# Performance work log

Hardware: AMD Instinct MI355X
Metric: run time of the kernel (lower is better)

## Reference

```python
import jax, jax.numpy as jnp
import numpy as np

H = 256          # hidden_size
S = 4            # feature size (2D -> 4)
T_OUT = 16       # args.output // args.skip
HT_LIM = 100.0   # hardtanh limit
B = 16384
OBS = 16


def lstm_cell(x, h, c, Wih, Whh, bih, bhh):
    # PyTorch gate order: i, f, g, o
    g = x @ Wih.T + h @ Whh.T + bih + bhh  # [B, 4H]
    i, f, gg, o = jnp.split(g, 4, axis=-1)
    c = jax.nn.sigmoid(f) * c + jax.nn.sigmoid(i) * jnp.tanh(gg)
    h = jax.nn.sigmoid(o) * jnp.tanh(c)
    return h, c


def encode(seq, Wih, Whh, bih, bhh):
    # seq: [B, T, S]; single-layer LSTM, return final (h, c)
    h0 = jnp.zeros((seq.shape[0], H), seq.dtype)
    def step(carry, x):
        h, c = carry
        return lstm_cell(x, h, c, Wih, Whh, bih, bhh), None
    (h, c), _ = jax.lax.scan(step, (h0, h0), jnp.swapaxes(seq, 0, 1))
    return h, c


def setup_inputs() -> dict:
    key = jax.random.key(0)
    ks = jax.random.split(key, 32)
    sc = 0.05
    def W(k, shape):
        return (jax.random.normal(k, shape, jnp.float32) * sc)
    inp = {
        'speed': jax.random.normal(ks[0], (B, OBS, S), jnp.float32),
        'pos': jax.random.normal(ks[1], (B, OBS, S), jnp.float32),
        # speed encoder LSTM
        'sp_Wih': W(ks[2], (4 * H, S)), 'sp_Whh': W(ks[3], (4 * H, H)),
        'sp_bih': W(ks[4], (4 * H,)), 'sp_bhh': W(ks[5], (4 * H,)),
        # pos encoder LSTM
        'po_Wih': W(ks[6], (4 * H, S)), 'po_Whh': W(ks[7], (4 * H, H)),
        'po_bih': W(ks[8], (4 * H,)), 'po_bhh': W(ks[9], (4 * H,)),
        # speed decoder LSTMCell
        'dsp_Wih': W(ks[10], (4 * H, S)), 'dsp_Whh': W(ks[11], (4 * H, H)),
        'dsp_bih': W(ks[12], (4 * H,)), 'dsp_bhh': W(ks[13], (4 * H,)),
        # crossing decoder LSTMCell
        'dcr_Wih': W(ks[14], (4 * H, S)), 'dcr_Whh': W(ks[15], (4 * H, H)),
        'dcr_bih': W(ks[16], (4 * H,)), 'dcr_bhh': W(ks[17], (4 * H,)),
        # heads
        'fc_speed_W': W(ks[18], (S, H)), 'fc_speed_b': W(ks[19], (S,)),
        'fc_cross_W': W(ks[20], (2, H)), 'fc_cross_b': W(ks[21], (2,)),
        'emb_W': W(ks[22], (S, H)), 'emb_b': W(ks[23], (S,)),
    }
    return inp


def reference(speed, pos,
              sp_Wih, sp_Whh, sp_bih, sp_bhh,
              po_Wih, po_Whh, po_bih, po_bhh,
              dsp_Wih, dsp_Whh, dsp_bih, dsp_bhh,
              dcr_Wih, dcr_Whh, dcr_bih, dcr_bhh,
              fc_speed_W, fc_speed_b, fc_cross_W, fc_cross_b,
              emb_W, emb_b):
    hsp, csp = encode(speed, sp_Wih, sp_Whh, sp_bih, sp_bhh)
    hpo, cpo = encode(pos, po_Wih, po_Whh, po_bih, po_bhh)
    h0 = hpo + hsp
    c0 = cpo + csp

    # ---- speed decoder: feed back hardtanh(fc_speed(h)) (detached) ----
    def sp_step(carry, _):
        h, c, x = carry
        h, c = lstm_cell(x, h, c, dsp_Wih, dsp_Whh, dsp_bih, dsp_bhh)
        out = jnp.clip(h @ fc_speed_W.T + fc_speed_b, -HT_LIM, HT_LIM)
        return (h, c, jax.lax.stop_gradient(out)), out
    _, sp_outs = jax.lax.scan(sp_step, (h0, c0, speed[:, -1, :]), None, length=T_OUT)
    speed_outputs = jnp.swapaxes(sp_outs, 0, 1)  # [B, T_OUT, S]

    # ---- crossing decoder: feed back relu(pos_embedding(h)) (detached) ----
    def cr_step(carry, _):
        h, c, x = carry
        h, c = lstm_cell(x, h, c, dcr_Wih, dcr_Whh, dcr_bih, dcr_bhh)
        logits = jax.nn.relu(h @ fc_cross_W.T + fc_cross_b)  # [B, 2]
        out = jax.nn.softmax(logits, axis=1)
        x_next = jax.lax.stop_gradient(jax.nn.relu(h @ emb_W.T + emb_b))
        return (h, c, x_next), out
    _, cr_outs = jax.lax.scan(cr_step, (h0, c0, pos[:, -1, :]), None, length=T_OUT)
    crossing_outputs = jnp.swapaxes(cr_outs, 0, 1)  # [B, T_OUT, 2]

    return (speed_outputs, crossing_outputs)
```

## Files before the change

kernel.cpp:

```cpp
#include <hip/hip_runtime.h>

typedef unsigned short ushort_t;
typedef __bf16 bf16x8 __attribute__((ext_vector_type(8)));
typedef float f32x4 __attribute__((ext_vector_type(4)));

#define PACK_W_ELEMS (8*9*8*512)
#define HEAD_ELEMS   (9*512)
#define PACK_TOTAL   (4*PACK_W_ELEMS + 2*HEAD_ELEMS)
#define FLAG_OFS     PACK_TOTAL

__device__ __forceinline__ float bf2f(ushort_t u){ return __uint_as_float(((unsigned)u)<<16); }
__device__ __forceinline__ ushort_t f2bf(float f){
  __bf16 h = (__bf16)f;
  return *(ushort_t*)&h;
}
__device__ __forceinline__ float rcp_(float x){ return __builtin_amdgcn_rcpf(x); }
__device__ __forceinline__ float sigmf_(float x){ return rcp_(1.0f + __expf(-x)); }
__device__ __forceinline__ float tanhf_(float x){ return 1.0f - 2.0f*rcp_(1.0f + __expf(2.0f*x)); }

__device__ __forceinline__ int sniff_f32(const ushort_t* w){
  int f32 = 0;
  #pragma unroll
  for (int i = 0; i < 32; ++i){
    float f = bf2f(w[2*i]);
    if (!(f > -8.f && f < 8.f)) f32 = 1;
  }
  return f32;
}
__device__ __forceinline__ float ldin(const ushort_t* p, int i, int f32){
  return f32 ? ((const float*)p)[i] : bf2f(p[i]);
}
__device__ __forceinline__ ushort_t ldw(const ushort_t* p, int i, int f32){
  return f32 ? f2bf(((const float*)p)[i]) : p[i];
}

struct PackArgs {
  const ushort_t* wih[4]; const ushort_t* whh[4];
  const ushort_t* bih[4]; const ushort_t* bhh[4];
  const ushort_t* fcsp_w; const ushort_t* fcsp_b;
  const ushort_t* fccr_w; const ushort_t* fccr_b;
  const ushort_t* emb_w;  const ushort_t* emb_b;
  ushort_t* ws;
};

__global__ void pack_kernel(PackArgs a){
  const int f32 = sniff_f32(a.whh[0]);
  int idx = blockIdx.x*256 + threadIdx.x;
  if (blockIdx.x == 0 && threadIdx.x == 0) *(int*)(a.ws + FLAG_OFS) = f32;
  const int total_w = 4*PACK_W_ELEMS;
  if (idx < total_w){
    int l = idx / PACK_W_ELEMS;
    int r = idx % PACK_W_ELEMS;
    int j = r & 7;
    int lane = (r>>3) & 63;
    int tile = r >> 9;
    int gu = tile & 7;
    int kt = (tile >> 3) % 9;
    int wv = tile / 72;
    int g = gu >> 1, u = gu & 1;
    int n = (g*16 + wv*2 + u)*16 + (lane & 15);
    int k = kt*32 + ((lane>>4)<<3) + j;
    ushort_t v = 0;
    if (k < 256)       v = ldw(a.whh[l], n*256 + k, f32);
    else if (k < 260)  v = ldw(a.wih[l], n*4 + (k-256), f32);
    else if (k == 260) v = f2bf(ldin(a.bih[l], n, f32) + ldin(a.bhh[l], n, f32));
    a.ws[l*PACK_W_ELEMS + r] = v;
    return;
  }
  idx -= total_w;
  if (idx < 2*HEAD_ELEMS){
    int which = idx / HEAD_ELEMS;
    int r = idx % HEAD_ELEMS;
    int j = r & 7; int lane = (r>>3)&63; int kt = r>>9;
    int n = lane & 15; int k = kt*32 + ((lane>>4)<<3) + j;
    ushort_t v = 0;
    if (which == 0){
      if (n < 4){
        if (k < 256)       v = ldw(a.fcsp_w, n*256 + k, f32);
        else if (k == 260) v = f2bf(ldin(a.fcsp_b, n, f32));
      }
    } else {
      if (n < 4){
        if (k < 256)       v = ldw(a.emb_w, n*256 + k, f32);
        else if (k == 260) v = f2bf(ldin(a.emb_b, n, f32));
      } else if (n < 6){
        if (k < 256)       v = ldw(a.fccr_w, (n-4)*256 + k, f32);
        else if (k == 260) v = f2bf(ldin(a.fccr_b, n-4, f32));
      }
    }
    a.ws[total_w + idx] = v;
  }
}

#define PRE4(bw, s0, s1, s2, s3)                \
  bf16x8 s0 = *(const bf16x8*)&(bw)[0*512];     \
  bf16x8 s1 = *(const bf16x8*)&(bw)[1*512];     \
  bf16x8 s2 = *(const bf16x8*)&(bw)[2*512];     \
  bf16x8 s3 = *(const bf16x8*)&(bw)[3*512];

__device__ __forceinline__ void gate_gemm(const ushort_t* __restrict__ Aln,
                                          const ushort_t* __restrict__ bw,
                                          f32x4 (&acc)[4][8], int lane,
                                          bf16x8 p0, bf16x8 p1, bf16x8 p2, bf16x8 p3){
  #pragma unroll
  for (int i = 0; i < 4; ++i)
    #pragma unroll
    for (int j = 0; j < 8; ++j) acc[i][j] = (f32x4){0.f,0.f,0.f,0.f};
  const ushort_t* bp = bw;
  #pragma unroll 1
  for (int kt = 0; kt < 9; ++kt){
    bf16x8 q0 = *(const bf16x8*)&bp[4*512];
    bf16x8 q1 = *(const bf16x8*)&bp[5*512];
    bf16x8 q2 = *(const bf16x8*)&bp[6*512];
    bf16x8 q3 = *(const bf16x8*)&bp[7*512];
    bf16x8 a0 = *(const bf16x8*)&Aln[(0*9+kt)*512];
    bf16x8 a1 = *(const bf16x8*)&Aln[(1*9+kt)*512];
    bf16x8 a2 = *(const bf16x8*)&Aln[(2*9+kt)*512];
    bf16x8 a3 = *(const bf16x8*)&Aln[(3*9+kt)*512];
    acc[0][0] = __builtin_amdgcn_mfma_f32_16x16x32_bf16(a0, p0, acc[0][0], 0, 0, 0);
    acc[1][0] = __builtin_amdgcn_mfma_f32_16x16x32_bf16(a1, p0, acc[1][0], 0, 0, 0);
    acc[2][0] = __builtin_amdgcn_mfma_f32_16x16x32_bf16(a2, p0, acc[2][0], 0, 0, 0);
    acc[3][0] = __builtin_amdgcn_mfma_f32_16x16x32_bf16(a3, p0, acc[3][0], 0, 0, 0);
    acc[0][1] = __builtin_amdgcn_mfma_f32_16x16x32_bf16(a0, p1, acc[0][1], 0, 0, 0);
    acc[1][1] = __builtin_amdgcn_mfma_f32_16x16x32_bf16(a1, p1, acc[1][1], 0, 0, 0);
    acc[2][1] = __builtin_amdgcn_mfma_f32_16x16x32_bf16(a2, p1, acc[2][1], 0, 0, 0);
    acc[3][1] = __builtin_amdgcn_mfma_f32_16x16x32_bf16(a3, p1, acc[3][1], 0, 0, 0);
    acc[0][2] = __builtin_amdgcn_mfma_f32_16x16x32_bf16(a0, p2, acc[0][2], 0, 0, 0);
    acc[1][2] = __builtin_amdgcn_mfma_f32_16x16x32_bf16(a1, p2, acc[1][2], 0, 0, 0);
    acc[2][2] = __builtin_amdgcn_mfma_f32_16x16x32_bf16(a2, p2, acc[2][2], 0, 0, 0);
    acc[3][2] = __builtin_amdgcn_mfma_f32_16x16x32_bf16(a3, p2, acc[3][2], 0, 0, 0);
    acc[0][3] = __builtin_amdgcn_mfma_f32_16x16x32_bf16(a0, p3, acc[0][3], 0, 0, 0);
    acc[1][3] = __builtin_amdgcn_mfma_f32_16x16x32_bf16(a1, p3, acc[1][3], 0, 0, 0);
    acc[2][3] = __builtin_amdgcn_mfma_f32_16x16x32_bf16(a2, p3, acc[2][3], 0, 0, 0);
    acc[3][3] = __builtin_amdgcn_mfma_f32_16x16x32_bf16(a3, p3, acc[3][3], 0, 0, 0);
    if (kt < 8){
      p0 = *(const bf16x8*)&bp[4096 + 0*512];
      p1 = *(const bf16x8*)&bp[4096 + 1*512];
      p2 = *(const bf16x8*)&bp[4096 + 2*512];
      p3 = *(const bf16x8*)&bp[4096 + 3*512];
    }
    acc[0][4] = __builtin_amdgcn_mfma_f32_16x16x32_bf16(a0, q0, acc[0][4], 0, 0, 0);
    acc[1][4] = __builtin_amdgcn_mfma_f32_16x16x32_bf16(a1, q0, acc[1][4], 0, 0, 0);
    acc[2][4] = __builtin_amdgcn_mfma_f32_16x16x32_bf16(a2, q0, acc[2][4], 0, 0, 0);
    acc[3][4] = __builtin_amdgcn_mfma_f32_16x16x32_bf16(a3, q0, acc[3][4], 0, 0, 0);
    acc[0][5] = __builtin_amdgcn_mfma_f32_16x16x32_bf16(a0, q1, acc[0][5], 0, 0, 0);
    acc[1][5] = __builtin_amdgcn_mfma_f32_16x16x32_bf16(a1, q1, acc[1][5], 0, 0, 0);
    acc[2][5] = __builtin_amdgcn_mfma_f32_16x16x32_bf16(a2, q1, acc[2][5], 0, 0, 0);
    acc[3][5] = __builtin_amdgcn_mfma_f32_16x16x32_bf16(a3, q1, acc[3][5], 0, 0, 0);
    acc[0][6] = __builtin_amdgcn_mfma_f32_16x16x32_bf16(a0, q2, acc[0][6], 0, 0, 0);
    acc[1][6] = __builtin_amdgcn_mfma_f32_16x16x32_bf16(a1, q2, acc[1][6], 0, 0, 0);
    acc[2][6] = __builtin_amdgcn_mfma_f32_16x16x32_bf16(a2, q2, acc[2][6], 0, 0, 0);
    acc[3][6] = __builtin_amdgcn_mfma_f32_16x16x32_bf16(a3, q2, acc[3][6], 0, 0, 0);
    acc[0][7] = __builtin_amdgcn_mfma_f32_16x16x32_bf16(a0, q3, acc[0][7], 0, 0, 0);
    acc[1][7] = __builtin_amdgcn_mfma_f32_16x16x32_bf16(a1, q3, acc[1][7], 0, 0, 0);
    acc[2][7] = __builtin_amdgcn_mfma_f32_16x16x32_bf16(a2, q3, acc[2][7], 0, 0, 0);
    acc[3][7] = __builtin_amdgcn_mfma_f32_16x16x32_bf16(a3, q3, acc[3][7], 0, 0, 0);
    bp += 4096;
  }
}

__device__ __forceinline__ void gates_wb(f32x4 (&acc)[4][8], float (&cw)[4][2][4],
                                         ushort_t* __restrict__ Ap, int wbBase){
  #pragma unroll
  for (int mt = 0; mt < 4; ++mt)
    #pragma unroll
    for (int u = 0; u < 2; ++u)
      #pragma unroll
      for (int r = 0; r < 4; ++r){
        const float i_ = acc[mt][u][r];
        const float f_ = acc[mt][2+u][r];
        const float g_ = acc[mt][4+u][r];
        const float o_ = acc[mt][6+u][r];
        const float ei = __expf(-i_);
        const float ef = __expf(-f_);
        const float eg = __expf(-2.0f*g_);
        const float di = 1.0f + ei, df = 1.0f + ef;
        const float dg = 1.0f + eg, ng = 1.0f - eg;
        const float dig = di*dg;
        const float cn = (cw[mt][u][r]*dig + ng*df) * rcp_(df*dig);
        const float eo = __expf(-o_);
        const float ec = __expf(-2.0f*cn);
        const float hn = (1.0f - ec) * rcp_((1.0f + eo)*(1.0f + ec));
        cw[mt][u][r] = cn;
        Ap[mt*4608 + u*256 + r*8 + wbBase] = f2bf(hn);
      }
}

__global__ __launch_bounds__(512, 2) void pvlstm_main(
    const ushort_t* __restrict__ ws,
    const ushort_t* __restrict__ speed,
    const ushort_t* __restrict__ pos,
    void* __restrict__ outv)
{
  __shared__ ushort_t ApS[4*9*512];
  __shared__ ushort_t ApP[4*9*512];
  __shared__ ushort_t xsS[64*64];
  __shared__ ushort_t xsP[64*64];
  __shared__ float    ostS[64*64];
  __shared__ float    ostC[64*32];

  const int f32   = *(const int*)(ws + FLAG_OFS);
  const int tid   = threadIdx.x;
  const int lane  = tid & 63;
  const int w     = tid >> 6;
  const int col16 = lane & 15;
  const int quad  = lane >> 4;
  const int brow0 = blockIdx.x * 64;
  const int wbBase = w*512 + (col16>>3)*128 + quad*32 + (col16&7);

  ushort_t* outu = (ushort_t*)outv;
  float*    outf = (float*)outv;

  const ushort_t* headsp = ws + 4*PACK_W_ELEMS;
  const ushort_t* headcr = headsp + HEAD_ELEMS;
  const ushort_t* aS  = ApS + lane*8;
  const ushort_t* aP  = ApP + lane*8;
  const ushort_t* bwS  = ws + 0*PACK_W_ELEMS + (size_t)w*36864 + (size_t)lane*8;
  const ushort_t* bwP  = ws + 1*PACK_W_ELEMS + (size_t)w*36864 + (size_t)lane*8;
  const ushort_t* bwDS = ws + 2*PACK_W_ELEMS + (size_t)w*36864 + (size_t)lane*8;
  const ushort_t* bwDC = ws + 3*PACK_W_ELEMS + (size_t)w*36864 + (size_t)lane*8;

  float cwA[4][2][4], cwB[4][2][4];
  f32x4 acc[4][8];

  for (int i = tid; i < 4096; i += 512){
    int gi = (brow0 + (i>>6))*64 + (i&63);
    xsS[i] = f2bf(ldin(speed, gi, f32));
    xsP[i] = f2bf(ldin(pos,   gi, f32));
  }
  for (int i = tid; i < 4*9*512/2; i += 512){
    ((unsigned*)ApS)[i] = 0u; ((unsigned*)ApP)[i] = 0u;
  }
  #pragma unroll
  for (int mt = 0; mt < 4; ++mt)
    #pragma unroll
    for (int u = 0; u < 2; ++u)
      #pragma unroll
      for (int r = 0; r < 4; ++r){ cwA[mt][u][r] = 0.f; cwB[mt][u][r] = 0.f; }
  __syncthreads();
  if (tid < 64){
    ushort_t* xpS = &ApS[((tid>>4)*9 + 8)*512 + (tid&15)*8];
    ushort_t* xpP = &ApP[((tid>>4)*9 + 8)*512 + (tid&15)*8];
    *(uint2*)xpS = *(const uint2*)&xsS[tid*64];
    xpS[4] = (ushort_t)0x3f80;
    xpP[4] = (ushort_t)0x3f80;
  }
  __syncthreads();

  for (int t = 0; t < 16; ++t){
    {
      PRE4(bwS, s0, s1, s2, s3)
      if (t > 0) gates_wb(acc, cwB, ApP, wbBase);
      if (tid < 64)
        *(uint2*)&ApP[((tid>>4)*9 + 8)*512 + (tid&15)*8] = *(const uint2*)&xsP[tid*64 + t*4];
      gate_gemm(aS, bwS, acc, lane, s0, s1, s2, s3);
    }
    __syncthreads();
    {
      PRE4(bwP, s0, s1, s2, s3)
      gates_wb(acc, cwA, ApS, wbBase);
      if (t < 15 && tid < 64)
        *(uint2*)&ApS[((tid>>4)*9 + 8)*512 + (tid&15)*8] = *(const uint2*)&xsS[tid*64 + t*4 + 4];
      gate_gemm(aP, bwP, acc, lane, s0, s1, s2, s3);
    }
    __syncthreads();
  }
  #pragma unroll
  for (int mt = 0; mt < 4; ++mt)
    #pragma unroll
    for (int u = 0; u < 2; ++u)
      #pragma unroll
      for (int r = 0; r < 4; ++r){
        const float i_ = acc[mt][u][r];
        const float f_ = acc[mt][2+u][r];
        const float g_ = acc[mt][4+u][r];
        const float o_ = acc[mt][6+u][r];
        const float ei = __expf(-i_);
        const float ef = __expf(-f_);
        const float eg = __expf(-2.0f*g_);
        const float di = 1.0f + ei, df = 1.0f + ef;
        const float dg = 1.0f + eg, ng = 1.0f - eg;
        const float dig = di*dg;
        const float cn = (cwB[mt][u][r]*dig + ng*df) * rcp_(df*dig);
        const float eo = __expf(-o_);
        const float ec = __expf(-2.0f*cn);
        const float hn = (1.0f - ec) * rcp_((1.0f + eo)*(1.0f + ec));
        const float c0 = cwA[mt][u][r] + cn;
        cwA[mt][u][r] = c0; cwB[mt][u][r] = c0;
        const int ad = mt*4608 + u*256 + r*8 + wbBase;
        ushort_t h0 = f2bf(bf2f(ApS[ad]) + hn);
        ApS[ad] = h0; ApP[ad] = h0;
      }
  if (tid < 64){
    *(uint2*)&ApS[((tid>>4)*9 + 8)*512 + (tid&15)*8] = *(const uint2*)&xsS[tid*64 + 60];
    *(uint2*)&ApP[((tid>>4)*9 + 8)*512 + (tid&15)*8] = *(const uint2*)&xsP[tid*64 + 60];
  }
  __syncthreads();

  for (int t = 0; t < 16; ++t){
    {
      PRE4(bwDS, s0, s1, s2, s3)
      if (t > 0 && w >= 4){
        const int mt = w - 4;
        f32x4 hacc = (f32x4){0.f,0.f,0.f,0.f};
        #pragma unroll
        for (int kt = 0; kt < 9; ++kt){
          bf16x8 a  = *(const bf16x8*)&aP[(mt*9+kt)*512];
          bf16x8 bv = *(const bf16x8*)&headcr[((size_t)kt*64 + lane)*8];
          hacc = __builtin_amdgcn_mfma_f32_16x16x32_bf16(a, bv, hacc, 0, 0, 0);
        }
        const int s = col16;
        #pragma unroll
        for (int r = 0; r < 4; ++r){
          float v = fmaxf(hacc[r], 0.f);
          const float o = __shfl_xor(v, 1, 64);
          const int m = mt*16 + quad*4 + r;
          if (s < 4){
            ApP[(mt*9+8)*512 + (m&15)*8 + s] = f2bf(v);
          } else if (s < 6){
            const float mx = fmaxf(v, o);
            const float e0 = __expf(v-mx), e1 = __expf(o-mx);
            ostC[m*32 + (t-1)*2 + (s-4)] = e0*rcp_(e0+e1);
          }
        }
      }
      gate_gemm(aS, bwDS, acc, lane, s0, s1, s2, s3);
    }
    __syncthreads();
    {
      PRE4(bwDC, s0, s1, s2, s3)
      gates_wb(acc, cwA, ApS, wbBase);
      gate_gemm(aP, bwDC, acc, lane, s0, s1, s2, s3);
    }
    __syncthreads();
    gates_wb(acc, cwB, ApP, wbBase);
    if (w < 4){
      const int mt = w;
      f32x4 hacc = (f32x4){0.f,0.f,0.f,0.f};
      #pragma unroll
      for (int kt = 0; kt < 9; ++kt){
        bf16x8 a  = *(const bf16x8*)&aS[(mt*9+kt)*512];
        bf16x8 bv = *(const bf16x8*)&headsp[((size_t)kt*64 + lane)*8];
        hacc = __builtin_amdgcn_mfma_f32_16x16x32_bf16(a, bv, hacc, 0, 0, 0);
      }
      const int s = col16;
      if (s < 4){
        #pragma unroll
        for (int r = 0; r < 4; ++r){
          float v = fminf(fmaxf(hacc[r], -100.f), 100.f);
          const int m = mt*16 + quad*4 + r;
          ostS[m*64 + t*4 + s] = v;
          ApS[(mt*9+8)*512 + (m&15)*8 + s] = f2bf(v);
        }
      }
    }
    __syncthreads();
  }
  if (w >= 4){
    const int mt = w - 4;
    f32x4 hacc = (f32x4){0.f,0.f,0.f,0.f};
    #pragma unroll
    for (int kt = 0; kt < 9; ++kt){
      bf16x8 a  = *(const bf16x8*)&aP[(mt*9+kt)*512];
      bf16x8 bv = *(const bf16x8*)&headcr[((size_t)kt*64 + lane)*8];
      hacc = __builtin_amdgcn_mfma_f32_16x16x32_bf16(a, bv, hacc, 0, 0, 0);
    }
    const int s = col16;
    if (s >= 4 && s < 6){
      #pragma unroll
      for (int r = 0; r < 4; ++r){
        float v = fmaxf(hacc[r], 0.f);
        const float o = __shfl_xor(v, 1, 64);
        const int m = mt*16 + quad*4 + r;
        const float mx = fmaxf(v, o);
        const float e0 = __expf(v-mx), e1 = __expf(o-mx);
        ostC[m*32 + 15*2 + (s-4)] = e0*rcp_(e0+e1);
      }
    }
  }
  __syncthreads();

  for (int i = tid; i < 4096; i += 512){
    const int oi = (brow0 + (i>>6))*64 + (i&63);
    const float v = ostS[i];
    if (f32) outf[oi] = v; else outu[oi] = f2bf(v);
  }
  for (int i = tid; i < 2048; i += 512){
    const int oi = 1048576 + (brow0 + (i>>5))*32 + (i&31);
    const float v = ostC[i];
    if (f32) outf[oi] = v; else outu[oi] = f2bf(v);
  }
}

extern "C" void kernel_launch(void* const* d_in, const int* in_sizes, int n_in,
                              void* d_out, int out_size, void* d_ws, size_t ws_size,
                              hipStream_t stream) {
  PackArgs pa;
  pa.wih[0]=(const ushort_t*)d_in[2];  pa.whh[0]=(const ushort_t*)d_in[3];
  pa.bih[0]=(const ushort_t*)d_in[4];  pa.bhh[0]=(const ushort_t*)d_in[5];
  pa.wih[1]=(const ushort_t*)d_in[6];  pa.whh[1]=(const ushort_t*)d_in[7];
  pa.bih[1]=(const ushort_t*)d_in[8];  pa.bhh[1]=(const ushort_t*)d_in[9];
  pa.wih[2]=(const ushort_t*)d_in[10]; pa.whh[2]=(const ushort_t*)d_in[11];
  pa.bih[2]=(const ushort_t*)d_in[12]; pa.bhh[2]=(const ushort_t*)d_in[13];
  pa.wih[3]=(const ushort_t*)d_in[14]; pa.whh[3]=(const ushort_t*)d_in[15];
  pa.bih[3]=(const ushort_t*)d_in[16]; pa.bhh[3]=(const ushort_t*)d_in[17];
  pa.fcsp_w=(const ushort_t*)d_in[18]; pa.fcsp_b=(const ushort_t*)d_in[19];
  pa.fccr_w=(const ushort_t*)d_in[20]; pa.fccr_b=(const ushort_t*)d_in[21];
  pa.emb_w =(const ushort_t*)d_in[22]; pa.emb_b =(const ushort_t*)d_in[23];
  pa.ws = (ushort_t*)d_ws;

  hipLaunchKernelGGL(pack_kernel, dim3((PACK_TOTAL + 255)/256), dim3(256), 0, stream, pa);
  hipLaunchKernelGGL(pvlstm_main, dim3(256), dim3(512), 0, stream,
      (const ushort_t*)d_ws,
      (const ushort_t*)d_in[0], (const ushort_t*)d_in[1],
      d_out);
}
```

Before: 827.4 us.

## Switch gate GEMMs from 16x16x32 to 32x32x16 MFMA with repacked layouts

Replaces the 16x16x32 bf16 MFMA tiling of the LSTM gate GEMMs with 32x32x16 MFMA tiles, repacking weights and the shared-memory hidden-state layout to match. Each wave now owns 2x4 accumulators of 16 floats over 18 K-steps instead of 4x8 accumulators of 4 floats over 9 K-steps. The aim is fewer MFMA issues and fewer A/B fragment loads per output. The head GEMMs, gate writeback and input-feed addressing are remapped to the new layout, which risks indexing errors and different LDS bank-conflict patterns.

```diff
diff --git a/kernel.cpp b/kernel.cpp
--- a/kernel.cpp
+++ b/kernel.cpp
@@ -3,8 +3,9 @@
 typedef unsigned short ushort_t;
 typedef __bf16 bf16x8 __attribute__((ext_vector_type(8)));
 typedef float f32x4 __attribute__((ext_vector_type(4)));
-
-#define PACK_W_ELEMS (8*9*8*512)
+typedef float f32x16 __attribute__((ext_vector_type(16)));
+
+#define PACK_W_ELEMS (8*18*4*512)
 #define HEAD_ELEMS   (9*512)
 #define PACK_TOTAL   (4*PACK_W_ELEMS + 2*HEAD_ELEMS)
 #define FLAG_OFS     PACK_TOTAL
@@ -15,8 +16,6 @@
   return *(ushort_t*)&h;
 }
 __device__ __forceinline__ float rcp_(float x){ return __builtin_amdgcn_rcpf(x); }
-__device__ __forceinline__ float sigmf_(float x){ return rcp_(1.0f + __expf(-x)); }
-__device__ __forceinline__ float tanhf_(float x){ return 1.0f - 2.0f*rcp_(1.0f + __expf(2.0f*x)); }
 
 __device__ __forceinline__ int sniff_f32(const ushort_t* w){
   int f32 = 0;
@@ -54,12 +53,11 @@
     int j = r & 7;
     int lane = (r>>3) & 63;
     int tile = r >> 9;
-    int gu = tile & 7;
-    int kt = (tile >> 3) % 9;
+    int g = tile & 3;
+    int kt = (tile >> 2) % 18;
     int wv = tile / 72;
-    int g = gu >> 1, u = gu & 1;
-    int n = (g*16 + wv*2 + u)*16 + (lane & 15);
-    int k = kt*32 + ((lane>>4)<<3) + j;
+    int n = g*256 + wv*32 + (lane & 31);
+    int k = kt*16 + ((lane>>5)<<3) + j;
     ushort_t v = 0;
     if (k < 256)       v = ldw(a.whh[l], n*256 + k, f32);
     else if (k < 260)  v = ldw(a.wih[l], n*4 + (k-256), f32);
@@ -100,90 +98,61 @@
 
 __device__ __forceinline__ void gate_gemm(const ushort_t* __restrict__ Aln,
                                           const ushort_t* __restrict__ bw,
-                                          f32x4 (&acc)[4][8], int lane,
+                                          f32x16 (&acc)[2][4],
                                           bf16x8 p0, bf16x8 p1, bf16x8 p2, bf16x8 p3){
   #pragma unroll
-  for (int i = 0; i < 4; ++i)
-    #pragma unroll
-    for (int j = 0; j < 8; ++j) acc[i][j] = (f32x4){0.f,0.f,0.f,0.f};
+  for (int i = 0; i < 2; ++i)
+    #pragma unroll
+    for (int j = 0; j < 4; ++j) acc[i][j] = (f32x16)(0.f);
   const ushort_t* bp = bw;
   #pragma unroll 1
-  for (int kt = 0; kt < 9; ++kt){
-    bf16x8 q0 = *(const bf16x8*)&bp[4*512];
-    bf16x8 q1 = *(const bf16x8*)&bp[5*512];
-    bf16x8 q2 = *(const bf16x8*)&bp[6*512];
-    bf16x8 q3 = *(const bf16x8*)&bp[7*512];
-    bf16x8 a0 = *(const bf16x8*)&Aln[(0*9+kt)*512];
-    bf16x8 a1 = *(const bf16x8*)&Aln[(1*9+kt)*512];
-    bf16x8 a2 = *(const bf16x8*)&Aln[(2*9+kt)*512];
-    bf16x8 a3 = *(const bf16x8*)&Aln[(3*9+kt)*512];
-    acc[0][0] = __builtin_amdgcn_mfma_f32_16x16x32_bf16(a0, p0, acc[0][0], 0, 0, 0);
-    acc[1][0] = __builtin_amdgcn_mfma_f32_16x16x32_bf16(a1, p0, acc[1][0], 0, 0, 0);
-    acc[2][0] = __builtin_amdgcn_mfma_f32_16x16x32_bf16(a2, p0, acc[2][0], 0, 0, 0);
-    acc[3][0] = __builtin_amdgcn_mfma_f32_16x16x32_bf16(a3, p0, acc[3][0], 0, 0, 0);
-    acc[0][1] = __builtin_amdgcn_mfma_f32_16x16x32_bf16(a0, p1, acc[0][1], 0, 0, 0);
-    acc[1][1] = __builtin_amdgcn_mfma_f32_16x16x32_bf16(a1, p1, acc[1][1], 0, 0, 0);
-    acc[2][1] = __builtin_amdgcn_mfma_f32_16x16x32_bf16(a2, p1, acc[2][1], 0, 0, 0);
-    acc[3][1] = __builtin_amdgcn_mfma_f32_16x16x32_bf16(a3, p1, acc[3][1], 0, 0, 0);
-    acc[0][2] = __builtin_amdgcn_mfma_f32_16x16x32_bf16(a0, p2, acc[0][2], 0, 0, 0);
-    acc[1][2] = __builtin_amdgcn_mfma_f32_16x16x32_bf16(a1, p2, acc[1][2], 0, 0, 0);
-    acc[2][2] = __builtin_amdgcn_mfma_f32_16x16x32_bf16(a2, p2, acc[2][2], 0, 0, 0);
-    acc[3][2] = __builtin_amdgcn_mfma_f32_16x16x32_bf16(a3, p2, acc[3][2], 0, 0, 0);
-    acc[0][3] = __builtin_amdgcn_mfma_f32_16x16x32_bf16(a0, p3, acc[0][3], 0, 0, 0);
-    acc[1][3] = __builtin_amdgcn_mfma_f32_16x16x32_bf16(a1, p3, acc[1][3], 0, 0, 0);
-    acc[2][3] = __builtin_amdgcn_mfma_f32_16x16x32_bf16(a2, p3, acc[2][3], 0, 0, 0);
-    acc[3][3] = __builtin_amdgcn_mfma_f32_16x16x32_bf16(a3, p3, acc[3][3], 0, 0, 0);
-    if (kt < 8){
-      p0 = *(const bf16x8*)&bp[4096 + 0*512];
-      p1 = *(const bf16x8*)&bp[4096 + 1*512];
-      p2 = *(const bf16x8*)&bp[4096 + 2*512];
-      p3 = *(const bf16x8*)&bp[4096 + 3*512];
-    }
-    acc[0][4] = __builtin_amdgcn_mfma_f32_16x16x32_bf16(a0, q0, acc[0][4], 0, 0, 0);
-    acc[1][4] = __builtin_amdgcn_mfma_f32_16x16x32_bf16(a1, q0, acc[1][4], 0, 0, 0);
-    acc[2][4] = __builtin_amdgcn_mfma_f32_16x16x32_bf16(a2, q0, acc[2][4], 0, 0, 0);
-    acc[3][4] = __builtin_amdgcn_mfma_f32_16x16x32_bf16(a3, q0, acc[3][4], 0, 0, 0);
-    acc[0][5] = __builtin_amdgcn_mfma_f32_16x16x32_bf16(a0, q1, acc[0][5], 0, 0, 0);
-    acc[1][5] = __builtin_amdgcn_mfma_f32_16x16x32_bf16(a1, q1, acc[1][5], 0, 0, 0);
-    acc[2][5] = __builtin_amdgcn_mfma_f32_16x16x32_bf16(a2, q1, acc[2][5], 0, 0, 0);
-    acc[3][5] = __builtin_amdgcn_mfma_f32_16x16x32_bf16(a3, q1, acc[3][5], 0, 0, 0);
-    acc[0][6] = __builtin_amdgcn_mfma_f32_16x16x32_bf16(a0, q2, acc[0][6], 0, 0, 0);
-    acc[1][6] = __builtin_amdgcn_mfma_f32_16x16x32_bf16(a1, q2, acc[1][6], 0, 0, 0);
-    acc[2][6] = __builtin_amdgcn_mfma_f32_16x16x32_bf16(a2, q2, acc[2][6], 0, 0, 0);
-    acc[3][6] = __builtin_amdgcn_mfma_f32_16x16x32_bf16(a3, q2, acc[3][6], 0, 0, 0);
-    acc[0][7] = __builtin_amdgcn_mfma_f32_16x16x32_bf16(a0, q3, acc[0][7], 0, 0, 0);
-    acc[1][7] = __builtin_amdgcn_mfma_f32_16x16x32_bf16(a1, q3, acc[1][7], 0, 0, 0);
-    acc[2][7] = __builtin_amdgcn_mfma_f32_16x16x32_bf16(a2, q3, acc[2][7], 0, 0, 0);
-    acc[3][7] = __builtin_amdgcn_mfma_f32_16x16x32_bf16(a3, q3, acc[3][7], 0, 0, 0);
-    bp += 4096;
-  }
-}
-
-__device__ __forceinline__ void gates_wb(f32x4 (&acc)[4][8], float (&cw)[4][2][4],
-                                         ushort_t* __restrict__ Ap, int wbBase){
-  #pragma unroll
-  for (int mt = 0; mt < 4; ++mt)
-    #pragma unroll
-    for (int u = 0; u < 2; ++u)
-      #pragma unroll
-      for (int r = 0; r < 4; ++r){
-        const float i_ = acc[mt][u][r];
-        const float f_ = acc[mt][2+u][r];
-        const float g_ = acc[mt][4+u][r];
-        const float o_ = acc[mt][6+u][r];
-        const float ei = __expf(-i_);
-        const float ef = __expf(-f_);
-        const float eg = __expf(-2.0f*g_);
-        const float di = 1.0f + ei, df = 1.0f + ef;
-        const float dg = 1.0f + eg, ng = 1.0f - eg;
-        const float dig = di*dg;
-        const float cn = (cw[mt][u][r]*dig + ng*df) * rcp_(df*dig);
-        const float eo = __expf(-o_);
-        const float ec = __expf(-2.0f*cn);
-        const float hn = (1.0f - ec) * rcp_((1.0f + eo)*(1.0f + ec));
-        cw[mt][u][r] = cn;
-        Ap[mt*4608 + u*256 + r*8 + wbBase] = f2bf(hn);
-      }
+  for (int kt = 0; kt < 18; ++kt){
+    bf16x8 a0 = *(const bf16x8*)&Aln[(     kt)*512];
+    bf16x8 a1 = *(const bf16x8*)&Aln[(18 + kt)*512];
+    acc[0][0] = __builtin_amdgcn_mfma_f32_32x32x16_bf16(a0, p0, acc[0][0], 0, 0, 0);
+    acc[1][0] = __builtin_amdgcn_mfma_f32_32x32x16_bf16(a1, p0, acc[1][0], 0, 0, 0);
+    acc[0][1] = __builtin_amdgcn_mfma_f32_32x32x16_bf16(a0, p1, acc[0][1], 0, 0, 0);
+    acc[1][1] = __builtin_amdgcn_mfma_f32_32x32x16_bf16(a1, p1, acc[1][1], 0, 0, 0);
+    bf16x8 q0, q1, q2, q3;
+    if (kt < 17){
+      q0 = *(const bf16x8*)&bp[2048 + 0*512];
+      q1 = *(const bf16x8*)&bp[2048 + 1*512];
+      q2 = *(const bf16x8*)&bp[2048 + 2*512];
+      q3 = *(const bf16x8*)&bp[2048 + 3*512];
+    }
+    acc[0][2] = __builtin_amdgcn_mfma_f32_32x32x16_bf16(a0, p2, acc[0][2], 0, 0, 0);
+    acc[1][2] = __builtin_amdgcn_mfma_f32_32x32x16_bf16(a1, p2, acc[1][2], 0, 0, 0);
+    acc[0][3] = __builtin_amdgcn_mfma_f32_32x32x16_bf16(a0, p3, acc[0][3], 0, 0, 0);
+    acc[1][3] = __builtin_amdgcn_mfma_f32_32x32x16_bf16(a1, p3, acc[1][3], 0, 0, 0);
+    if (kt < 17){ p0 = q0; p1 = q1; p2 = q2; p3 = q3; }
+    bp += 2048;
+  }
+}
+
+__device__ __forceinline__ void gates_wb(f32x16 (&acc)[2][4], float (&cw)[2][16],
+                                         ushort_t* __restrict__ Ap, int wbBase, int hi5){
+  #pragma unroll
+  for (int mt = 0; mt < 2; ++mt)
+    #pragma unroll
+    for (int reg = 0; reg < 16; ++reg){
+      const float i_ = acc[mt][0][reg];
+      const float f_ = acc[mt][1][reg];
+      const float g_ = acc[mt][2][reg];
+      const float o_ = acc[mt][3][reg];
+      const float ei = __expf(-i_);
+      const float ef = __expf(-f_);
+      const float eg = __expf(-2.0f*g_);
+      const float di = 1.0f + ei, df = 1.0f + ef;
+      const float dg = 1.0f + eg, ng = 1.0f - eg;
+      const float dig = di*dg;
+      const float cn = (cw[mt][reg]*dig + ng*df) * rcp_(df*dig);
+      const float eo = __expf(-o_);
+      const float ec = __expf(-2.0f*cn);
+      const float hn = (1.0f - ec) * rcp_((1.0f + eo)*(1.0f + ec));
+      cw[mt][reg] = cn;
+      const int rw = (reg&3) + 8*(reg>>2) + 4*hi5;
+      Ap[mt*9216 + wbBase + rw*8] = f2bf(hn);
+    }
 }
 
 __global__ __launch_bounds__(512, 2) void pvlstm_main(
@@ -192,8 +161,8 @@
     const ushort_t* __restrict__ pos,
     void* __restrict__ outv)
 {
-  __shared__ ushort_t ApS[4*9*512];
-  __shared__ ushort_t ApP[4*9*512];
+  __shared__ ushort_t ApS[2*18*512];
+  __shared__ ushort_t ApP[2*18*512];
   __shared__ ushort_t xsS[64*64];
   __shared__ ushort_t xsP[64*64];
   __shared__ float    ostS[64*64];
@@ -205,8 +174,10 @@
   const int w     = tid >> 6;
   const int col16 = lane & 15;
   const int quad  = lane >> 4;
+  const int c5    = lane & 31;
+  const int hi5   = lane >> 5;
   const int brow0 = blockIdx.x * 64;
-  const int wbBase = w*512 + (col16>>3)*128 + quad*32 + (col16&7);
+  const int wbBase = (w*2 + (c5>>4))*512 + ((c5>>3)&1)*256 + (lane & 7);
 
   ushort_t* outu = (ushort_t*)outv;
   float*    outf = (float*)outv;
@@ -220,27 +191,25 @@
   const ushort_t* bwDS = ws + 2*PACK_W_ELEMS + (size_t)w*36864 + (size_t)lane*8;
   const ushort_t* bwDC = ws + 3*PACK_W_ELEMS + (size_t)w*36864 + (size_t)lane*8;
 
-  float cwA[4][2][4], cwB[4][2][4];
-  f32x4 acc[4][8];
+  float cwA[2][16], cwB[2][16];
+  f32x16 acc[2][4];
 
   for (int i = tid; i < 4096; i += 512){
     int gi = (brow0 + (i>>6))*64 + (i&63);
     xsS[i] = f2bf(ldin(speed, gi, f32));
     xsP[i] = f2bf(ldin(pos,   gi, f32));
   }
-  for (int i = tid; i < 4*9*512/2; i += 512){
+  for (int i = tid; i < 2*18*512/2; i += 512){
     ((unsigned*)ApS)[i] = 0u; ((unsigned*)ApP)[i] = 0u;
   }
   #pragma unroll
-  for (int mt = 0; mt < 4; ++mt)
-    #pragma unroll
-    for (int u = 0; u < 2; ++u)
-      #pragma unroll
-      for (int r = 0; r < 4; ++r){ cwA[mt][u][r] = 0.f; cwB[mt][u][r] = 0.f; }
+  for (int mt = 0; mt < 2; ++mt)
+    #pragma unroll
+    for (int r = 0; r < 16; ++r){ cwA[mt][r] = 0.f; cwB[mt][r] = 0.f; }
   __syncthreads();
   if (tid < 64){
-    ushort_t* xpS = &ApS[((tid>>4)*9 + 8)*512 + (tid&15)*8];
-    ushort_t* xpP = &ApP[((tid>>4)*9 + 8)*512 + (tid&15)*8];
+    ushort_t* xpS = &ApS[((tid>>5)*18 + 16)*512 + (tid&31)*8];
+    ushort_t* xpP = &ApP[((tid>>5)*18 + 16)*512 + (tid&31)*8];
     *(uint2*)xpS = *(const uint2*)&xsS[tid*64];
     xpS[4] = (ushort_t)0x3f80;
     xpP[4] = (ushort_t)0x3f80;
@@ -250,50 +219,49 @@
   for (int t = 0; t < 16; ++t){
     {
       PRE4(bwS, s0, s1, s2, s3)
-      if (t > 0) gates_wb(acc, cwB, ApP, wbBase);
+      if (t > 0) gates_wb(acc, cwB, ApP, wbBase, hi5);
       if (tid < 64)
-        *(uint2*)&ApP[((tid>>4)*9 + 8)*512 + (tid&15)*8] = *(const uint2*)&xsP[tid*64 + t*4];
-      gate_gemm(aS, bwS, acc, lane, s0, s1, s2, s3);
+        *(uint2*)&ApP[((tid>>5)*18 + 16)*512 + (tid&31)*8] = *(const uint2*)&xsP[tid*64 + t*4];
+      gate_gemm(aS, bwS, acc, s0, s1, s2, s3);
     }
     __syncthreads();
     {
       PRE4(bwP, s0, s1, s2, s3)
-      gates_wb(acc, cwA, ApS, wbBase);
+      gates_wb(acc, cwA, ApS, wbBase, hi5);
       if (t < 15 && tid < 64)
-        *(uint2*)&ApS[((tid>>4)*9 + 8)*512 + (tid&15)*8] = *(const uint2*)&xsS[tid*64 + t*4 + 4];
-      gate_gemm(aP, bwP, acc, lane, s0, s1, s2, s3);
-    }
-    __syncthreads();
-  }
-  #pragma unroll
-  for (int mt = 0; mt < 4; ++mt)
-    #pragma unroll
-    for (int u = 0; u < 2; ++u)
-      #pragma unroll
-      for (int r = 0; r < 4; ++r){
-        const float i_ = acc[mt][u][r];
-        const float f_ = acc[mt][2+u][r];
-        const float g_ = acc[mt][4+u][r];
-        const float o_ = acc[mt][6+u][r];
-        const float ei = __expf(-i_);
-        const float ef = __expf(-f_);
-        const float eg = __expf(-2.0f*g_);
-        const float di = 1.0f + ei, df = 1.0f + ef;
-        const float dg = 1.0f + eg, ng = 1.0f - eg;
-        const float dig = di*dg;
-        const float cn = (cwB[mt][u][r]*dig + ng*df) * rcp_(df*dig);
-        const float eo = __expf(-o_);
-        const float ec = __expf(-2.0f*cn);
-        const float hn = (1.0f - ec) * rcp_((1.0f + eo)*(1.0f + ec));
-        const float c0 = cwA[mt][u][r] + cn;
-        cwA[mt][u][r] = c0; cwB[mt][u][r] = c0;
-        const int ad = mt*4608 + u*256 + r*8 + wbBase;
-        ushort_t h0 = f2bf(bf2f(ApS[ad]) + hn);
-        ApS[ad] = h0; ApP[ad] = h0;
-      }
+        *(uint2*)&ApS[((tid>>5)*18 + 16)*512 + (tid&31)*8] = *(const uint2*)&xsS[tid*64 + t*4 + 4];
+      gate_gemm(aP, bwP, acc, s0, s1, s2, s3);
+    }
+    __syncthreads();
+  }
+  #pragma unroll
+  for (int mt = 0; mt < 2; ++mt)
+    #pragma unroll
+    for (int reg = 0; reg < 16; ++reg){
+      const float i_ = acc[mt][0][reg];
+      const float f_ = acc[mt][1][reg];
+      const float g_ = acc[mt][2][reg];
+      const float o_ = acc[mt][3][reg];
+      const float ei = __expf(-i_);
+      const float ef = __expf(-f_);
+      const float eg = __expf(-2.0f*g_);
+      const float di = 1.0f + ei, df = 1.0f + ef;
+      const float dg = 1.0f + eg, ng = 1.0f - eg;
+      const float dig = di*dg;
+      const float cn = (cwB[mt][reg]*dig + ng*df) * rcp_(df*dig);
+      const float eo = __expf(-o_);
+      const float ec = __expf(-2.0f*cn);
+      const float hn = (1.0f - ec) * rcp_((1.0f + eo)*(1.0f + ec));
+      const float c0 = cwA[mt][reg] + cn;
+      cwA[mt][reg] = c0; cwB[mt][reg] = c0;
+      const int rw = (reg&3) + 8*(reg>>2) + 4*hi5;
+      const int ad = mt*9216 + wbBase + rw*8;
+      ushort_t h0 = f2bf(bf2f(ApS[ad]) + hn);
+      ApS[ad] = h0; ApP[ad] = h0;
+    }
   if (tid < 64){
-    *(uint2*)&ApS[((tid>>4)*9 + 8)*512 + (tid&15)*8] = *(const uint2*)&xsS[tid*64 + 60];
-    *(uint2*)&ApP[((tid>>4)*9 + 8)*512 + (tid&15)*8] = *(const uint2*)&xsP[tid*64 + 60];
+    *(uint2*)&ApS[((tid>>5)*18 + 16)*512 + (tid&31)*8] = *(const uint2*)&xsS[tid*64 + 60];
+    *(uint2*)&ApP[((tid>>5)*18 + 16)*512 + (tid&31)*8] = *(const uint2*)&xsP[tid*64 + 60];
   }
   __syncthreads();
 
@@ -302,10 +270,11 @@
       PRE4(bwDS, s0, s1, s2, s3)
       if (t > 0 && w >= 4){
         const int mt = w - 4;
+        const int hbase = ((mt>>1)*18 + hi5)*512 + ((quad&1)*256) + ((mt&1)*16 + col16)*8;
         f32x4 hacc = (f32x4){0.f,0.f,0.f,0.f};
         #pragma unroll
         for (int kt = 0; kt < 9; ++kt){
-          bf16x8 a  = *(const bf16x8*)&aP[(mt*9+kt)*512];
+          bf16x8 a  = *(const bf16x8*)&ApP[hbase + kt*1024];
           bf16x8 bv = *(const bf16x8*)&headcr[((size_t)kt*64 + lane)*8];
           hacc = __builtin_amdgcn_mfma_f32_16x16x32_bf16(a, bv, hacc, 0, 0, 0);
         }
@@ -316,7 +285,7 @@
           const float o = __shfl_xor(v, 1, 64);
           const int m = mt*16 + quad*4 + r;
           if (s < 4){
-            ApP[(mt*9+8)*512 + (m&15)*8 + s] = f2bf(v);
+            ApP[((m>>5)*18 + 16)*512 + (m&31)*8 + s] = f2bf(v);
           } else if (s < 6){
             const float mx = fmaxf(v, o);
             const float e0 = __expf(v-mx), e1 = __expf(o-mx);
@@ -324,22 +293,23 @@
           }
         }
       }
-      gate_gemm(aS, bwDS, acc, lane, s0, s1, s2, s3);
+      gate_gemm(aS, bwDS, acc, s0, s1, s2, s3);
     }
     __syncthreads();
     {
       PRE4(bwDC, s0, s1, s2, s3)
-      gates_wb(acc, cwA, ApS, wbBase);
-      gate_gemm(aP, bwDC, acc, lane, s0, s1, s2, s3);
-    }
-    __syncthreads();
-    gates_wb(acc, cwB, ApP, wbBase);
+      gates_wb(acc, cwA, ApS, wbBase, hi5);
+      gate_gemm(aP, bwDC, acc, s0, s1, s2, s3);
+    }
+    __syncthreads();
+    gates_wb(acc, cwB, ApP, wbBase, hi5);
     if (w < 4){
       const int mt = w;
+      const int hbase = ((mt>>1)*18 + hi5)*512 + ((quad&1)*256) + ((mt&1)*16 + col16)*8;
       f32x4 hacc = (f32x4){0.f,0.f,0.f,0.f};
       #pragma unroll
       for (int kt = 0; kt < 9; ++kt){
-        bf16x8 a  = *(const bf16x8*)&aS[(mt*9+kt)*512];
+        bf16x8 a  = *(const bf16x8*)&ApS[hbase + kt*1024];
         bf16x8 bv = *(const bf16x8*)&headsp[((size_t)kt*64 + lane)*8];
         hacc = __builtin_amdgcn_mfma_f32_16x16x32_bf16(a, bv, hacc, 0, 0, 0);
       }
@@ -350,7 +320,7 @@
           float v = fminf(fmaxf(hacc[r], -100.f), 100.f);
           const int m = mt*16 + quad*4 + r;
           ostS[m*64 + t*4 + s] = v;
-          ApS[(mt*9+8)*512 + (m&15)*8 + s] = f2bf(v);
+          ApS[((m>>5)*18 + 16)*512 + (m&31)*8 + s] = f2bf(v);
         }
       }
     }
@@ -358,10 +328,11 @@
   }
   if (w >= 4){
     const int mt = w - 4;
+    const int hbase = ((mt>>1)*18 + hi5)*512 + ((quad&1)*256) + ((mt&1)*16 + col16)*8;
     f32x4 hacc = (f32x4){0.f,0.f,0.f,0.f};
     #pragma unroll
     for (int kt = 0; kt < 9; ++kt){
-      bf16x8 a  = *(const bf16x8*)&aP[(mt*9+kt)*512];
+      bf16x8 a  = *(const bf16x8*)&ApP[hbase + kt*1024];
       bf16x8 bv = *(const bf16x8*)&headcr[((size_t)kt*64 + lane)*8];
       hacc = __builtin_amdgcn_mfma_f32_16x16x32_bf16(a, bv, hacc, 0, 0, 0);
     }
```

Result: slower. 910.0 us (+10.0%).
